# Kernel optimization log

Measured on AMD Instinct MI355X. Metric: run time of the kernel, lower is better.

## Reference

```python
import jax, jax.numpy as jnp
import numpy as np

B, C, IMG, P, D, H, L, FF, NC = 32, 3, 224, 16, 768, 12, 12, 3072, 14
G = IMG // P            # 14 patches per side
S = G * G + 1           # 197 tokens incl cls
DH = D // H             # 64 head dim


def layer_norm(x, w, b, eps=1e-5):
    m = jnp.mean(x, axis=-1, keepdims=True)
    v = jnp.mean((x - m) ** 2, axis=-1, keepdims=True)
    return (x - m) / jnp.sqrt(v + eps) * w + b


def setup_inputs() -> dict:
    key = jax.random.key(0)
    ks = iter(jax.random.split(key, 32))
    n = lambda s, scale=0.02: jax.random.normal(next(ks), s, dtype=jnp.float32) * scale
    inp = {
        'x': jax.random.normal(next(ks), (B, C, IMG, IMG), dtype=jnp.float32),
        'patch_w': n((D, C, P, P)),
        'patch_b': jnp.zeros((D,), jnp.float32),
        'cls_token': n((1, 1, D)),
        'pos_emb': n((1, S, D)),
        'ln1_w': jnp.ones((L, D), jnp.float32),
        'ln1_b': jnp.zeros((L, D), jnp.float32),
        'wq': n((L, D, D)), 'bq': jnp.zeros((L, D), jnp.float32),
        'wk': n((L, D, D)), 'bk': jnp.zeros((L, D), jnp.float32),
        'wv': n((L, D, D)), 'bv': jnp.zeros((L, D), jnp.float32),
        'wo': n((L, D, D)), 'bo': jnp.zeros((L, D), jnp.float32),
        'ln2_w': jnp.ones((L, D), jnp.float32),
        'ln2_b': jnp.zeros((L, D), jnp.float32),
        'fc1_w': n((L, FF, D)), 'fc1_b': jnp.zeros((L, FF), jnp.float32),
        'fc2_w': n((L, D, FF)), 'fc2_b': jnp.zeros((L, D), jnp.float32),
        'clf_w': n((NC, D)), 'clf_b': jnp.zeros((NC,), jnp.float32),
    }
    return inp


def _vit_forward(x, patch_w, patch_b, cls_token, pos_emb,
                 ln1_w, ln1_b, wq, bq, wk, bk, wv, bv, wo, bo,
                 ln2_w, ln2_b, fc1_w, fc1_b, fc2_w, fc2_b, clf_w, clf_b):
    b = x.shape[0]
    # Patch embed: stride==kernel conv == reshape to patches + matmul.
    patches = x.reshape(b, C, G, P, G, P).transpose(0, 2, 4, 1, 3, 5).reshape(b, G * G, C * P * P)
    emb = patches @ patch_w.reshape(D, -1).T + patch_b            # [b, 196, D]
    h = jnp.concatenate([jnp.broadcast_to(cls_token, (b, 1, D)), emb], axis=1) + pos_emb

    def block(h, p):
        l1w, l1b, Wq, Bq, Wk, Bk, Wv, Bv, Wo, Bo, l2w, l2b, F1w, F1b, F2w, F2b = p
        y = layer_norm(h, l1w, l1b)
        q = (y @ Wq.T + Bq).reshape(b, S, H, DH)
        k = (y @ Wk.T + Bk).reshape(b, S, H, DH)
        v = (y @ Wv.T + Bv).reshape(b, S, H, DH)
        scores = jnp.einsum('bqhd,bkhd->bhqk', q, k) / np.sqrt(DH).astype(np.float32)
        a = jax.nn.softmax(scores, axis=-1)
        o = jnp.einsum('bhqk,bkhd->bqhd', a, v).reshape(b, S, D)
        h = h + (o @ Wo.T + Bo)
        y = layer_norm(h, l2w, l2b)
        h = h + jax.nn.gelu(y @ F1w.T + F1b, approximate=False) @ F2w.T + F2b
        return h, None

    params = (ln1_w, ln1_b, wq, bq, wk, bk, wv, bv, wo, bo,
              ln2_w, ln2_b, fc1_w, fc1_b, fc2_w, fc2_b)
    h, _ = jax.lax.scan(block, h, params)
    logits = h[:, 0] @ clf_w.T + clf_b                            # [b, NC]
    return logits


def reference(x, patch_w, patch_b, cls_token, pos_emb,
              ln1_w, ln1_b, wq, bq, wk, bk, wv, bv, wo, bo,
              ln2_w, ln2_b, fc1_w, fc1_b, fc2_w, fc2_b, clf_w, clf_b):
    return _vit_forward(x, patch_w, patch_b, cls_token, pos_emb,
                        ln1_w, ln1_b, wq, bq, wk, bk, wv, bv, wo, bo,
                        ln2_w, ln2_b, fc1_w, fc1_b, fc2_w, fc2_b, clf_w, clf_b)
```

## Files before the change

kernel.cpp:

```cpp
#include <hip/hip_runtime.h>
#include <hip/hip_bf16.h>
#include <cstdint>
#include <cstddef>

typedef __attribute__((ext_vector_type(8))) short  bf16x8;
typedef __attribute__((ext_vector_type(4))) float  f32x4;
typedef __attribute__((ext_vector_type(4))) ushort u16x4;
typedef __attribute__((ext_vector_type(8))) ushort u16x8;

#define MFMA16(a, b, c) __builtin_amdgcn_mfma_f32_16x16x32_bf16((a), (b), (c), 0, 0, 0)

__device__ __forceinline__ ushort f2b(float x) {
    union { float f; uint32_t u; } c; c.f = x;
    uint32_t u = c.u + 0x7fffu + ((c.u >> 16) & 1u);
    return (ushort)(u >> 16);
}

__device__ __forceinline__ void gload_lds16(const ushort* g, ushort* l) {
    __builtin_amdgcn_global_load_lds((const __attribute__((address_space(1))) void*)g,
                                     (__attribute__((address_space(3))) void*)l, 16, 0, 0);
}

template<int BN, int OUTBF, int RES, int GELU>
__global__ __launch_bounds__(256)
void gemm_bt(const ushort* __restrict__ A, const ushort* __restrict__ W,
             const float* __restrict__ bias, const float* resid,
             void* outp, int M, int N, int K, int gx)
{
    constexpr int NJ  = BN / 32;
    constexpr int NCH = 8 + BN / 16;
    constexpr int PER = NCH / 4;
    __shared__ __align__(16) ushort Als[2][128 * 32];
    __shared__ __align__(16) ushort Bls[2][BN * 32];

    const int tid  = threadIdx.x;
    const int lane = tid & 63, wid = tid >> 6;

    const int nwg  = gridDim.x;
    const int orig = blockIdx.x;
    const int xcd = orig & 7, local = orig >> 3;
    const int q8 = nwg >> 3, r8 = nwg & 7;
    const int swz = (xcd < r8 ? xcd * (q8 + 1) : r8 * (q8 + 1) + (xcd - r8) * q8) + local;
    const int bx = swz % gx, by = swz / gx;

    const int m0 = by * 128, n0 = bx * BN;
    const int wr = wid >> 1, wc = wid & 1;
    const int ecol = lane & 15, eg = lane >> 4;
    const int lr = lane >> 2;
    const int lc = (lane & 3) * 8;

    f32x4 acc[4][NJ] = {};

    auto stage = [&](int p, int k0) {
#pragma unroll
        for (int c = 0; c < PER; ++c) {
            const int q = wid * PER + c;
            if (q < 8) {
                const int row = q * 16 + lr;
                int ga = m0 + row; if (ga > M - 1) ga = M - 1;
                gload_lds16(A + (size_t)ga * K + k0 + lc, &Als[p][q * 512]);
            } else {
                const int qq = q - 8;
                const int row = qq * 16 + lr;
                gload_lds16(W + (size_t)(n0 + row) * K + k0 + lc, &Bls[p][qq * 512]);
            }
        }
    };

    const int NT = K >> 5;
    stage(0, 0);
    __syncthreads();

    int cur = 0;
    for (int t = 0; t < NT; ++t) {
        if (t + 1 < NT) stage(cur ^ 1, (t + 1) << 5);
        bf16x8 af[4], bfr[NJ];
#pragma unroll
        for (int i = 0; i < 4; ++i)
            af[i] = *(const bf16x8*)&Als[cur][(wr * 64 + i * 16 + ecol) * 32 + eg * 8];
#pragma unroll
        for (int j = 0; j < NJ; ++j)
            bfr[j] = *(const bf16x8*)&Bls[cur][(wc * (BN / 2) + j * 16 + ecol) * 32 + eg * 8];
#pragma unroll
        for (int i = 0; i < 4; ++i)
#pragma unroll
            for (int j = 0; j < NJ; ++j)
                acc[i][j] = MFMA16(af[i], bfr[j], acc[i][j]);
        if (t + 1 < NT) __syncthreads();
        cur ^= 1;
    }

#pragma unroll
    for (int i = 0; i < 4; ++i) {
        const int mb = m0 + wr * 64 + i * 16 + eg * 4;
#pragma unroll
        for (int j = 0; j < NJ; ++j) {
            const int n = n0 + wc * (BN / 2) + j * 16 + ecol;
            const float bv = bias[n];
#pragma unroll
            for (int r = 0; r < 4; ++r) {
                const int m = mb + r;
                if (m < M) {
                    float v = acc[i][j][r] + bv;
                    if (RES)  v += resid[(size_t)m * N + n];
                    if (GELU) v = 0.5f * v * (1.0f + erff(v * 0.70710678118f));
                    if (OUTBF) ((ushort*)outp)[(size_t)m * N + n] = f2b(v);
                    else       ((float*)outp)[(size_t)m * N + n]  = v;
                }
            }
        }
    }
}

__global__ __launch_bounds__(256)
void attn_k(const ushort* __restrict__ qkv, ushort* __restrict__ o)
{
    __shared__ __align__(16) ushort Vt[64][224];
    __shared__ __align__(16) ushort Pb[4][16][224];
    const int bh = blockIdx.x;
    const int b = bh / 12, hh = bh % 12;
    const int tid = threadIdx.x, lane = tid & 63, wid = tid >> 6;
    const size_t rs = 2304;
    const ushort* qb = qkv + (size_t)b * 197 * rs + hh * 64;
    const ushort* kb = qb + 768;
    const ushort* vb = qb + 1536;

    for (int i = tid; i < 197 * 64; i += 256) {
        const int s = i >> 6, d = i & 63;
        Vt[d][s] = vb[(size_t)s * rs + d];
    }
    for (int i = tid; i < 64 * 27; i += 256) {
        const int d = i / 27, s = 197 + i % 27;
        Vt[d][s] = 0;
    }
    __syncthreads();

    const int ecol = lane & 15, eg = lane >> 4;
    const bool m12bad = (192 + ecol) > 196;

    for (int qt = wid; qt < 13; qt += 4) {
        int qrow = qt * 16 + ecol; if (qrow > 196) qrow = 196;
        bf16x8 qa0 = *(const bf16x8*)&qb[(size_t)qrow * rs + eg * 8];
        bf16x8 qa1 = *(const bf16x8*)&qb[(size_t)qrow * rs + 32 + eg * 8];

        f32x4 s[13];
#pragma unroll
        for (int kt = 0; kt < 13; ++kt) {
            int krow = kt * 16 + ecol; if (krow > 196) krow = 196;
            bf16x8 kf0 = *(const bf16x8*)&kb[(size_t)krow * rs + eg * 8];
            bf16x8 kf1 = *(const bf16x8*)&kb[(size_t)krow * rs + 32 + eg * 8];
            f32x4 a = {};
            a = MFMA16(qa0, kf0, a);
            a = MFMA16(qa1, kf1, a);
            s[kt] = a;
        }
#pragma unroll
        for (int kt = 0; kt < 13; ++kt)
#pragma unroll
            for (int r = 0; r < 4; ++r) s[kt][r] *= 0.125f;
        if (m12bad) { s[12][0] = -1e30f; s[12][1] = -1e30f; s[12][2] = -1e30f; s[12][3] = -1e30f; }

#pragma unroll
        for (int r = 0; r < 4; ++r) {
            float mx = s[0][r];
#pragma unroll
            for (int kt = 1; kt < 13; ++kt) mx = fmaxf(mx, s[kt][r]);
#pragma unroll
            for (int off = 1; off < 16; off <<= 1) mx = fmaxf(mx, __shfl_xor(mx, off));
            float sm = 0.0f;
#pragma unroll
            for (int kt = 0; kt < 13; ++kt) { float e = __expf(s[kt][r] - mx); s[kt][r] = e; sm += e; }
#pragma unroll
            for (int off = 1; off < 16; off <<= 1) sm += __shfl_xor(sm, off);
            const float inv = 1.0f / sm;
#pragma unroll
            for (int kt = 0; kt < 13; ++kt) s[kt][r] *= inv;
        }

#pragma unroll
        for (int kt = 0; kt < 13; ++kt)
#pragma unroll
            for (int r = 0; r < 4; ++r)
                Pb[wid][eg * 4 + r][kt * 16 + ecol] = f2b(s[kt][r]);
#pragma unroll
        for (int r = 0; r < 4; ++r) Pb[wid][eg * 4 + r][208 + ecol] = 0;
        asm volatile("s_waitcnt lgkmcnt(0)" ::: "memory");
        __builtin_amdgcn_sched_barrier(0);

        f32x4 oacc[4] = {};
#pragma unroll
        for (int ks = 0; ks < 7; ++ks) {
            bf16x8 pa = *(const bf16x8*)&Pb[wid][ecol][ks * 32 + eg * 8];
#pragma unroll
            for (int dt = 0; dt < 4; ++dt) {
                bf16x8 vf = *(const bf16x8*)&Vt[dt * 16 + ecol][ks * 32 + eg * 8];
                oacc[dt] = MFMA16(pa, vf, oacc[dt]);
            }
        }
#pragma unroll
        for (int dt = 0; dt < 4; ++dt)
#pragma unroll
            for (int r = 0; r < 4; ++r) {
                const int q = qt * 16 + eg * 4 + r;
                if (q < 197)
                    o[((size_t)(b * 197 + q)) * 768 + hh * 64 + dt * 16 + ecol] = f2b(oacc[dt][r]);
            }
        asm volatile("s_waitcnt lgkmcnt(0)" ::: "memory");
        __builtin_amdgcn_sched_barrier(0);
    }
}

__global__ __launch_bounds__(256)
void ln_k(const float* __restrict__ x, const float* __restrict__ g,
          const float* __restrict__ bta, ushort* __restrict__ y, int rows)
{
    const int row  = blockIdx.x * 4 + (threadIdx.x >> 6);
    const int lane = threadIdx.x & 63;
    if (row >= rows) return;
    const float* xr = x + (size_t)row * 768;
    f32x4 v[3];
#pragma unroll
    for (int t = 0; t < 3; ++t) v[t] = *(const f32x4*)&xr[(lane + t * 64) * 4];
    float s = 0.0f;
#pragma unroll
    for (int t = 0; t < 3; ++t) s += v[t][0] + v[t][1] + v[t][2] + v[t][3];
#pragma unroll
    for (int off = 1; off < 64; off <<= 1) s += __shfl_xor(s, off);
    const float mean = s * (1.0f / 768.0f);
    float sq = 0.0f;
#pragma unroll
    for (int t = 0; t < 3; ++t)
#pragma unroll
        for (int c = 0; c < 4; ++c) { const float d = v[t][c] - mean; sq += d * d; }
#pragma unroll
    for (int off = 1; off < 64; off <<= 1) sq += __shfl_xor(sq, off);
    const float rstd = rsqrtf(sq * (1.0f / 768.0f) + 1e-5f);
    ushort* yr = y + (size_t)row * 768;
#pragma unroll
    for (int t = 0; t < 3; ++t) {
        const int c0 = (lane + t * 64) * 4;
        f32x4 gw = *(const f32x4*)&g[c0];
        f32x4 bb = *(const f32x4*)&bta[c0];
        u16x4 ov;
#pragma unroll
        for (int c = 0; c < 4; ++c) ov[c] = f2b((v[t][c] - mean) * rstd * gw[c] + bb[c]);
        *(u16x4*)&yr[c0] = ov;
    }
}

__global__ void im2col_k(const float* __restrict__ x, ushort* __restrict__ p)
{
    const int gid = blockIdx.x * 256 + threadIdx.x;
    if (gid >= 6272 * 768) return;
    const int m = gid / 768, idx = gid - m * 768;
    const int b = m / 196, t = m - b * 196;
    const int gy = t / 14, gx = t - gy * 14;
    const int c = idx >> 8, rr = idx & 255;
    const int py = rr >> 4, px = rr & 15;
    const float v = x[(((size_t)(b * 3 + c) * 224) + gy * 16 + py) * 224 + gx * 16 + px];
    p[gid] = f2b(v);
}

__global__ void assemble_k(const float* __restrict__ emb, const float* __restrict__ cls,
                           const float* __restrict__ pos, float* __restrict__ h)
{
    const int gid = blockIdx.x * 256 + threadIdx.x;
    if (gid >= 6304 * 192) return;
    const int r = gid / 192, c4 = gid - r * 192;
    const int b = r / 197, s = r - b * 197;
    f32x4 pe = *(const f32x4*)&pos[(s * 192 + c4) * 4];
    f32x4 sv;
    if (s == 0) sv = *(const f32x4*)&cls[c4 * 4];
    else        sv = *(const f32x4*)&emb[((size_t)(b * 196 + (s - 1)) * 192 + c4) * 4];
    f32x4 ov = pe + sv;
    *(f32x4*)&h[(size_t)gid * 4] = ov;
}

__global__ void cvt_k(const float* __restrict__ src, ushort* __restrict__ dst, int n8)
{
    const int g = blockIdx.x * 256 + threadIdx.x;
    if (g >= n8) return;
    const int e = g * 8;
    f32x4 a = *(const f32x4*)&src[e];
    f32x4 b = *(const f32x4*)&src[e + 4];
    u16x8 ov;
#pragma unroll
    for (int c = 0; c < 4; ++c) { ov[c] = f2b(a[c]); ov[4 + c] = f2b(b[c]); }
    *(u16x8*)&dst[e] = ov;
}

__global__ void conv6_k(const float* __restrict__ s0, const float* __restrict__ s1,
                        const float* __restrict__ s2, const float* __restrict__ s3,
                        const float* __restrict__ s4, const float* __restrict__ s5,
                        ushort* __restrict__ dst)
{
    const int g = blockIdx.x * 256 + threadIdx.x;
    if (g >= 884736) return;
    const int e = g * 8;
    const float* src; int off;
    if      (e < 589824)  { src = s0; off = e; }
    else if (e < 1179648) { src = s1; off = e - 589824; }
    else if (e < 1769472) { src = s2; off = e - 1179648; }
    else if (e < 2359296) { src = s3; off = e - 1769472; }
    else if (e < 4718592) { src = s4; off = e - 2359296; }
    else                  { src = s5; off = e - 4718592; }
    f32x4 a = *(const f32x4*)&src[off];
    f32x4 b = *(const f32x4*)&src[off + 4];
    u16x8 ov;
#pragma unroll
    for (int c = 0; c < 4; ++c) { ov[c] = f2b(a[c]); ov[4 + c] = f2b(b[c]); }
    *(u16x8*)&dst[e] = ov;
}

__global__ void bias3_k(const float* __restrict__ b0, const float* __restrict__ b1,
                        const float* __restrict__ b2, float* __restrict__ dst)
{
    const int i = blockIdx.x * 256 + threadIdx.x;
    if (i >= 2304) return;
    dst[i] = (i < 768) ? b0[i] : (i < 1536 ? b1[i - 768] : b2[i - 1536]);
}

__global__ __launch_bounds__(64)
void clf_k(const float* __restrict__ h, const float* __restrict__ w,
           const float* __restrict__ bias, float* __restrict__ out)
{
    const int b = blockIdx.x, lane = threadIdx.x;
    const float* hr = h + (size_t)b * 197 * 768;
    float hv[12];
#pragma unroll
    for (int j = 0; j < 12; ++j) hv[j] = hr[lane + j * 64];
    for (int n = 0; n < 14; ++n) {
        float sm = 0.0f;
#pragma unroll
        for (int j = 0; j < 12; ++j) sm += hv[j] * w[n * 768 + lane + j * 64];
#pragma unroll
        for (int off = 1; off < 64; off <<= 1) sm += __shfl_xor(sm, off);
        if (lane == 0) out[b * 14 + n] = sm + bias[n];
    }
}

extern "C" void kernel_launch(void* const* d_in, const int* in_sizes, int n_in,
                              void* d_out, int out_size, void* d_ws, size_t ws_size,
                              hipStream_t stream)
{
    const float* x       = (const float*)d_in[0];
    const float* patch_w = (const float*)d_in[1];
    const float* patch_b = (const float*)d_in[2];
    const float* cls_tok = (const float*)d_in[3];
    const float* pos_emb = (const float*)d_in[4];
    const float* ln1_w   = (const float*)d_in[5];
    const float* ln1_b   = (const float*)d_in[6];
    const float* wq      = (const float*)d_in[7];
    const float* bq      = (const float*)d_in[8];
    const float* wk      = (const float*)d_in[9];
    const float* bk      = (const float*)d_in[10];
    const float* wv      = (const float*)d_in[11];
    const float* bv      = (const float*)d_in[12];
    const float* wo      = (const float*)d_in[13];
    const float* bo      = (const float*)d_in[14];
    const float* ln2_w   = (const float*)d_in[15];
    const float* ln2_b   = (const float*)d_in[16];
    const float* fc1w    = (const float*)d_in[17];
    const float* fc1b    = (const float*)d_in[18];
    const float* fc2w    = (const float*)d_in[19];
    const float* fc2b    = (const float*)d_in[20];
    const float* clfw    = (const float*)d_in[21];
    const float* clfb    = (const float*)d_in[22];

    char* ws = (char*)d_ws;
    float*  h    = (float*)(ws + 0);
    ushort* y    = (ushort*)(ws + 19365888);
    ushort* qkv  = (ushort*)(ws + 29048832);
    ushort* o    = (ushort*)(ws + 58097664);
    ushort* ff   = (ushort*)(ws + 67780608);
    ushort* wbuf = (ushort*)(ws + 106512384);
    float*  b3   = (float*)(ws + 120668160);
    ushort* patches = (ushort*)(ws + 67780608);
    float*  emb     = (float*)(ws + 67780608 + 16777216);

    im2col_k<<<18816, 256, 0, stream>>>(x, patches);
    cvt_k<<<288, 256, 0, stream>>>(patch_w, wbuf, 73728);
    gemm_bt<64, 0, 0, 0><<<12 * 49, 256, 0, stream>>>(patches, wbuf, patch_b,
                                                      (const float*)nullptr, (void*)emb, 6272, 768, 768, 12);
    assemble_k<<<4728, 256, 0, stream>>>(emb, cls_tok, pos_emb, h);

    for (int l = 0; l < 12; ++l) {
        conv6_k<<<3456, 256, 0, stream>>>(wq + (size_t)l * 589824, wk + (size_t)l * 589824,
                                          wv + (size_t)l * 589824, wo + (size_t)l * 589824,
                                          fc1w + (size_t)l * 2359296, fc2w + (size_t)l * 2359296, wbuf);
        bias3_k<<<9, 256, 0, stream>>>(bq + l * 768, bk + l * 768, bv + l * 768, b3);
        ln_k<<<1576, 256, 0, stream>>>(h, ln1_w + l * 768, ln1_b + l * 768, y, 6304);
        gemm_bt<128, 1, 0, 0><<<18 * 50, 256, 0, stream>>>(y, wbuf, b3,
                                                           (const float*)nullptr, (void*)qkv, 6304, 2304, 768, 18);
        attn_k<<<384, 256, 0, stream>>>(qkv, o);
        gemm_bt<64, 0, 1, 0><<<12 * 50, 256, 0, stream>>>(o, wbuf + 1769472, bo + l * 768,
                                                          (const float*)h, (void*)h, 6304, 768, 768, 12);
        ln_k<<<1576, 256, 0, stream>>>(h, ln2_w + l * 768, ln2_b + l * 768, y, 6304);
        gemm_bt<128, 1, 0, 1><<<24 * 50, 256, 0, stream>>>(y, wbuf + 2359296, fc1b + (size_t)l * 3072,
                                                           (const float*)nullptr, (void*)ff, 6304, 3072, 768, 24);
        gemm_bt<64, 0, 1, 0><<<12 * 50, 256, 0, stream>>>(ff, wbuf + 4718592, fc2b + l * 768,
                                                          (const float*)h, (void*)h, 6304, 768, 3072, 12);
    }
    clf_k<<<32, 64, 0, stream>>>(h, clfw, clfb, (float*)d_out);
}
```

Baseline: 3.408 ms.

## Triple-buffer GEMM LDS staging with vmcnt waits and fragment-ordered layout

Replaces the double-buffered A/B LDS tiles with a unified triple buffer and prefetches two K-steps ahead. Each iteration waits with a partial s_waitcnt vmcnt and a single barrier instead of two syncthreads. The staging lane mapping changes so each lane's 16-byte chunk lands where the MFMA fragment read expects it, which makes LDS reads contiguous per lane (lane*8) and avoids bank conflicts. The cost is more LDS per block, which may lower occupancy. Correctness also depends on the vmcnt count matching the number of outstanding loads.

Measured after the change: 4.283 ms. +25.7%, slower.

```diff
diff --git a/kernel.cpp b/kernel.cpp
--- a/kernel.cpp
+++ b/kernel.cpp
@@ -30,8 +30,7 @@
     constexpr int NJ  = BN / 32;
     constexpr int NCH = 8 + BN / 16;
     constexpr int PER = NCH / 4;
-    __shared__ __align__(16) ushort Als[2][128 * 32];
-    __shared__ __align__(16) ushort Bls[2][BN * 32];
+    __shared__ __align__(16) ushort LS[3][NCH * 512];
 
     const int tid  = threadIdx.x;
     const int lane = tid & 63, wid = tid >> 6;
@@ -46,8 +45,8 @@
     const int m0 = by * 128, n0 = bx * BN;
     const int wr = wid >> 1, wc = wid & 1;
     const int ecol = lane & 15, eg = lane >> 4;
-    const int lr = lane >> 2;
-    const int lc = (lane & 3) * 8;
+    const int srow = lane & 15;
+    const int scol = (lane >> 4) * 8;
 
     f32x4 acc[4][NJ] = {};
 
@@ -56,38 +55,38 @@
         for (int c = 0; c < PER; ++c) {
             const int q = wid * PER + c;
             if (q < 8) {
-                const int row = q * 16 + lr;
+                const int row = q * 16 + srow;
                 int ga = m0 + row; if (ga > M - 1) ga = M - 1;
-                gload_lds16(A + (size_t)ga * K + k0 + lc, &Als[p][q * 512]);
+                gload_lds16(A + (size_t)ga * K + k0 + scol, &LS[p][q * 512]);
             } else {
-                const int qq = q - 8;
-                const int row = qq * 16 + lr;
-                gload_lds16(W + (size_t)(n0 + row) * K + k0 + lc, &Bls[p][qq * 512]);
+                const int row = (q - 8) * 16 + srow;
+                gload_lds16(W + (size_t)(n0 + row) * K + k0 + scol, &LS[p][q * 512]);
             }
         }
     };
 
     const int NT = K >> 5;
     stage(0, 0);
-    __syncthreads();
-
-    int cur = 0;
+    stage(1, 32);
+
     for (int t = 0; t < NT; ++t) {
-        if (t + 1 < NT) stage(cur ^ 1, (t + 1) << 5);
+        if (t + 1 < NT) asm volatile("s_waitcnt vmcnt(%0)" :: "n"(PER) : "memory");
+        else            asm volatile("s_waitcnt vmcnt(0)" ::: "memory");
+        __builtin_amdgcn_s_barrier();
+        const int cur = t % 3;
+        if (t + 2 < NT) stage((t + 2) % 3, (t + 2) << 5);
         bf16x8 af[4], bfr[NJ];
 #pragma unroll
         for (int i = 0; i < 4; ++i)
-            af[i] = *(const bf16x8*)&Als[cur][(wr * 64 + i * 16 + ecol) * 32 + eg * 8];
+            af[i] = *(const bf16x8*)&LS[cur][(wr * 4 + i) * 512 + lane * 8];
 #pragma unroll
         for (int j = 0; j < NJ; ++j)
-            bfr[j] = *(const bf16x8*)&Bls[cur][(wc * (BN / 2) + j * 16 + ecol) * 32 + eg * 8];
+            bfr[j] = *(const bf16x8*)&LS[cur][(8 + wc * NJ + j) * 512 + lane * 8];
 #pragma unroll
         for (int i = 0; i < 4; ++i)
 #pragma unroll
             for (int j = 0; j < NJ; ++j)
                 acc[i][j] = MFMA16(af[i], bfr[j], acc[i][j]);
-        if (t + 1 < NT) __syncthreads();
-        cur ^= 1;
     }
 
 #pragma unroll
```

## Split-K with atomic accumulation for narrow N=768 GEMMs

Applied to the files above, without the earlier changes.

Adds a split-K mode to the bf16 GEMM, with each K-half accumulating into the fp32 output through atomic adds. The residual add is folded in by accumulating directly into h, and the patch-embed output is zeroed beforehand with a memset. The aim is to double the workgroup count for the N=768 GEMMs (patch embed, out-proj, FC2), which had only ~600 tiles and underfilled the GPU. In exchange it pays for atomic read-modify-write traffic, and the fp32 summation order becomes nondeterministic.

Result: slower. 3.771 ms (+10.6%).

```diff
diff --git a/kernel.cpp b/kernel.cpp
--- a/kernel.cpp
+++ b/kernel.cpp
@@ -21,11 +21,11 @@
                                      (__attribute__((address_space(3))) void*)l, 16, 0, 0);
 }
 
-template<int BN, int OUTBF, int RES, int GELU>
+template<int BN, int OUTBF, int RES, int GELU, int SPLITK, int ATOMIC>
 __global__ __launch_bounds__(256)
 void gemm_bt(const ushort* __restrict__ A, const ushort* __restrict__ W,
              const float* __restrict__ bias, const float* resid,
-             void* outp, int M, int N, int K, int gx)
+             void* outp, int M, int N, int K, int gx, int gy)
 {
     constexpr int NJ  = BN / 32;
     constexpr int NCH = 8 + BN / 16;
@@ -41,7 +41,12 @@
     const int xcd = orig & 7, local = orig >> 3;
     const int q8 = nwg >> 3, r8 = nwg & 7;
     const int swz = (xcd < r8 ? xcd * (q8 + 1) : r8 * (q8 + 1) + (xcd - r8) * q8) + local;
-    const int bx = swz % gx, by = swz / gx;
+    const int bx = swz % gx;
+    const int rem = swz / gx;
+    const int by = (SPLITK > 1) ? (rem % gy) : rem;
+    const int sk = (SPLITK > 1) ? (rem / gy) : 0;
+    const int Ks = K / SPLITK;
+    const int kb = sk * Ks;
 
     const int m0 = by * 128, n0 = bx * BN;
     const int wr = wid >> 1, wc = wid & 1;
@@ -58,16 +63,16 @@
             if (q < 8) {
                 const int row = q * 16 + lr;
                 int ga = m0 + row; if (ga > M - 1) ga = M - 1;
-                gload_lds16(A + (size_t)ga * K + k0 + lc, &Als[p][q * 512]);
+                gload_lds16(A + (size_t)ga * K + kb + k0 + lc, &Als[p][q * 512]);
             } else {
                 const int qq = q - 8;
                 const int row = qq * 16 + lr;
-                gload_lds16(W + (size_t)(n0 + row) * K + k0 + lc, &Bls[p][qq * 512]);
+                gload_lds16(W + (size_t)(n0 + row) * K + kb + k0 + lc, &Bls[p][qq * 512]);
             }
         }
     };
 
-    const int NT = K >> 5;
+    const int NT = Ks >> 5;
     stage(0, 0);
     __syncthreads();
 
@@ -96,16 +101,20 @@
 #pragma unroll
         for (int j = 0; j < NJ; ++j) {
             const int n = n0 + wc * (BN / 2) + j * 16 + ecol;
-            const float bv = bias[n];
+            const float bv = (ATOMIC && sk > 0) ? 0.0f : bias[n];
 #pragma unroll
             for (int r = 0; r < 4; ++r) {
                 const int m = mb + r;
                 if (m < M) {
                     float v = acc[i][j][r] + bv;
-                    if (RES)  v += resid[(size_t)m * N + n];
-                    if (GELU) v = 0.5f * v * (1.0f + erff(v * 0.70710678118f));
-                    if (OUTBF) ((ushort*)outp)[(size_t)m * N + n] = f2b(v);
-                    else       ((float*)outp)[(size_t)m * N + n]  = v;
+                    if (ATOMIC) {
+                        unsafeAtomicAdd(&((float*)outp)[(size_t)m * N + n], v);
+                    } else {
+                        if (RES)  v += resid[(size_t)m * N + n];
+                        if (GELU) v = 0.5f * v * (1.0f + erff(v * 0.70710678118f));
+                        if (OUTBF) ((ushort*)outp)[(size_t)m * N + n] = f2b(v);
+                        else       ((float*)outp)[(size_t)m * N + n]  = v;
+                    }
                 }
             }
         }
@@ -380,8 +389,9 @@
 
     im2col_k<<<18816, 256, 0, stream>>>(x, patches);
     cvt_k<<<288, 256, 0, stream>>>(patch_w, wbuf, 73728);
-    gemm_bt<64, 0, 0, 0><<<12 * 49, 256, 0, stream>>>(patches, wbuf, patch_b,
-                                                      (const float*)nullptr, (void*)emb, 6272, 768, 768, 12);
+    hipMemsetAsync(emb, 0, (size_t)6272 * 768 * 4, stream);
+    gemm_bt<64, 0, 0, 0, 2, 1><<<12 * 49 * 2, 256, 0, stream>>>(patches, wbuf, patch_b,
+                                                      (const float*)nullptr, (void*)emb, 6272, 768, 768, 12, 49);
     assemble_k<<<4728, 256, 0, stream>>>(emb, cls_tok, pos_emb, h);
 
     for (int l = 0; l < 12; ++l) {
@@ -390,16 +400,16 @@
                                           fc1w + (size_t)l * 2359296, fc2w + (size_t)l * 2359296, wbuf);
         bias3_k<<<9, 256, 0, stream>>>(bq + l * 768, bk + l * 768, bv + l * 768, b3);
         ln_k<<<1576, 256, 0, stream>>>(h, ln1_w + l * 768, ln1_b + l * 768, y, 6304);
-        gemm_bt<128, 1, 0, 0><<<18 * 50, 256, 0, stream>>>(y, wbuf, b3,
-                                                           (const float*)nullptr, (void*)qkv, 6304, 2304, 768, 18);
+        gemm_bt<128, 1, 0, 0, 1, 0><<<18 * 50, 256, 0, stream>>>(y, wbuf, b3,
+                                                           (const float*)nullptr, (void*)qkv, 6304, 2304, 768, 18, 50);
         attn_k<<<384, 256, 0, stream>>>(qkv, o);
-        gemm_bt<64, 0, 1, 0><<<12 * 50, 256, 0, stream>>>(o, wbuf + 1769472, bo + l * 768,
-                                                          (const float*)h, (void*)h, 6304, 768, 768, 12);
+        gemm_bt<64, 0, 0, 0, 2, 1><<<12 * 50 * 2, 256, 0, stream>>>(o, wbuf + 1769472, bo + l * 768,
+                                                          (const float*)nullptr, (void*)h, 6304, 768, 768, 12, 50);
         ln_k<<<1576, 256, 0, stream>>>(h, ln2_w + l * 768, ln2_b + l * 768, y, 6304);
-        gemm_bt<128, 1, 0, 1><<<24 * 50, 256, 0, stream>>>(y, wbuf + 2359296, fc1b + (size_t)l * 3072,
-                                                           (const float*)nullptr, (void*)ff, 6304, 3072, 768, 24);
-        gemm_bt<64, 0, 1, 0><<<12 * 50, 256, 0, stream>>>(ff, wbuf + 4718592, fc2b + l * 768,
-                                                          (const float*)h, (void*)h, 6304, 768, 3072, 12);
+        gemm_bt<128, 1, 0, 1, 1, 0><<<24 * 50, 256, 0, stream>>>(y, wbuf + 2359296, fc1b + (size_t)l * 3072,
+                                                           (const float*)nullptr, (void*)ff, 6304, 3072, 768, 24, 50);
+        gemm_bt<64, 0, 0, 0, 2, 1><<<12 * 50 * 2, 256, 0, stream>>>(ff, wbuf + 4718592, fc2b + l * 768,
+                                                          (const float*)nullptr, (void*)h, 6304, 768, 3072, 12, 50);
     }
     clf_k<<<32, 64, 0, stream>>>(h, clfw, clfb, (float*)d_out);
 }
```
